# Kernel tuning notes

Measured on AMD Instinct MI355X. Metric: run time of the kernel, lower is better.

The kernel has to match this reference:

```python
import jax, jax.numpy as jnp
import numpy as np

B, T, C, H = 4, 2048, 512, 8
HS = C // H  # head_size = 64
EPS = 1e-5


def layernorm(x, g, b):
    mu = jnp.mean(x, axis=-1, keepdims=True)
    var = jnp.mean(jnp.square(x - mu), axis=-1, keepdims=True)
    return (x - mu) * jax.lax.rsqrt(var + EPS) * g + b


def setup_inputs() -> dict:
    key = jax.random.key(0)
    ks = jax.random.split(key, 12)
    s_attn = 1.0 / np.sqrt(C)
    s_ff1 = 1.0 / np.sqrt(C)
    s_ff2 = 1.0 / np.sqrt(4 * C)
    return {
        "x": jax.random.normal(ks[0], (B, T, C), jnp.float32),
        "wq": jax.random.normal(ks[1], (H, C, HS), jnp.float32) * s_attn,
        "wk": jax.random.normal(ks[2], (H, C, HS), jnp.float32) * s_attn,
        "wv": jax.random.normal(ks[3], (H, C, HS), jnp.float32) * s_attn,
        "w1": jax.random.normal(ks[4], (C, 4 * C), jnp.float32) * s_ff1,
        "b1": jnp.zeros((4 * C,), jnp.float32),
        "w2": jax.random.normal(ks[5], (4 * C, C), jnp.float32) * s_ff2,
        "b2": jnp.zeros((C,), jnp.float32),
        "ln1_g": jnp.ones((C,), jnp.float32),
        "ln1_b": jnp.zeros((C,), jnp.float32),
        "ln2_g": jnp.ones((C,), jnp.float32),
        "ln2_b": jnp.zeros((C,), jnp.float32),
    }


def reference(x, wq, wk, wv, w1, b1, w2, b2, ln1_g, ln1_b, ln2_g, ln2_b):
    # pre-LN multi-head causal self-attention
    h = layernorm(x, ln1_g, ln1_b)                       # [B,T,C]
    q = jnp.einsum("btc,hcd->bhtd", h, wq)
    k = jnp.einsum("btc,hcd->bhtd", h, wk)
    v = jnp.einsum("btc,hcd->bhtd", h, wv)
    # NOTE: source scales by full embed dim C, not head_size
    scores = jnp.einsum("bhtd,bhsd->bhts", q, k) * (C ** -0.5)  # [B,H,T,T]
    causal = jnp.tril(jnp.ones((T, T), bool))
    scores = jnp.where(causal, scores, -jnp.inf)
    att = jax.nn.softmax(scores, axis=-1)
    out = jnp.einsum("bhts,bhsd->bhtd", att, v)          # [B,H,T,HS]
    out = out.transpose(0, 2, 1, 3).reshape(B, T, C)     # concat heads
    x = x + out
    # FFN with residual
    h2 = layernorm(x, ln2_g, ln2_b)
    ff = jax.nn.relu(h2 @ w1 + b1) @ w2 + b2
    return x + ff
```

## Files before the change

kernel.cpp:

```cpp
#include <hip/hip_runtime.h>

typedef unsigned short ushort_t;
typedef __attribute__((ext_vector_type(8))) short short8;
typedef __attribute__((ext_vector_type(4))) float floatx4;

#define B_  4
#define T_  2048
#define C_  512
#define H_  8
#define HS_ 64
#define M_  (B_*T_)
#define SCALE2 0.06376140168547404f

__device__ __forceinline__ float b2f(ushort_t u) {
  union { unsigned int i; float f; } w; w.i = ((unsigned int)u) << 16; return w.f;
}
__device__ __forceinline__ ushort_t f2b(float f) {
  union { float f; unsigned int i; } w; w.f = f;
  unsigned int x = w.i;
  return (ushort_t)((x + 0x7fffu + ((x >> 16) & 1u)) >> 16);
}
__device__ __forceinline__ unsigned int cvtpk(float a, float b) {
  unsigned int r;
  asm("v_cvt_pk_bf16_f32 %0, %1, %2" : "=v"(r) : "v"(a), "v"(b));
  return r;
}
__device__ __forceinline__ void gl_lds16(const ushort_t* g, ushort_t* l) {
  __builtin_amdgcn_global_load_lds((const unsigned int*)g, (unsigned int*)l, 16, 0, 0);
}

__global__ __launch_bounds__(256) void transpose_all(const float* __restrict__ wq,
                                                     const float* __restrict__ wk,
                                                     const float* __restrict__ wv,
                                                     const float* __restrict__ w1,
                                                     const float* __restrict__ w2,
                                                     ushort_t* __restrict__ qkvt,
                                                     ushort_t* __restrict__ w1t,
                                                     ushort_t* __restrict__ w2t) {
  __shared__ ushort_t t[32][33];
  int idx = blockIdx.x;
  const float* in; ushort_t* out; int K, N, bx, by, z = 0;
  float scl = (idx < 256) ? SCALE2 : 1.0f;
  if (idx < 768) {
    int seg = idx >> 8, li = idx & 255;
    in = seg == 0 ? wq : (seg == 1 ? wk : wv);
    out = qkvt + (size_t)seg * 262144;
    K = 512; N = 64;
    z = li >> 5; li &= 31;
    bx = li & 1; by = li >> 1;
  } else if (idx < 1792) {
    int li = idx - 768;
    in = w1; out = w1t; K = 512; N = 2048;
    bx = li & 63; by = li >> 6;
  } else {
    int li = idx - 1792;
    in = w2; out = w2t; K = 2048; N = 512;
    bx = li & 15; by = li >> 4;
  }
  size_t zoff = (size_t)z * K * N;
  int n0 = bx * 32, k0 = by * 32;
  int tx = threadIdx.x & 31, ty = threadIdx.x >> 5;
#pragma unroll
  for (int i = 0; i < 4; i++)
    t[ty + 8 * i][tx] = f2b(in[zoff + (size_t)(k0 + ty + 8 * i) * N + n0 + tx] * scl);
  __syncthreads();
#pragma unroll
  for (int i = 0; i < 4; i++)
    out[zoff + (size_t)(n0 + ty + 8 * i) * K + k0 + tx] = t[tx][ty + 8 * i];
}

__global__ __launch_bounds__(256) void ln_k(const float* __restrict__ X,
                                            const float* __restrict__ g,
                                            const float* __restrict__ bb,
                                            ushort_t* __restrict__ Y) {
  int wave = threadIdx.x >> 6, lane = threadIdx.x & 63;
  size_t row = (size_t)blockIdx.x * 4 + wave;
  float v[8], s = 0.f, s2 = 0.f;
#pragma unroll
  for (int i = 0; i < 8; i++) {
    float x = X[row * C_ + lane + 64 * i];
    v[i] = x; s += x; s2 += x * x;
  }
#pragma unroll
  for (int off = 32; off >= 1; off >>= 1) {
    s += __shfl_xor(s, off); s2 += __shfl_xor(s2, off);
  }
  float mu = s * (1.0f / C_);
  float var = s2 * (1.0f / C_) - mu * mu;
  float rs = rsqrtf(var + 1e-5f);
  ushort_t* yr = Y + row * C_;
#pragma unroll
  for (int i = 0; i < 8; i++) {
    int c = lane + 64 * i;
    yr[c] = f2b((v[i] - mu) * rs * g[c] + bb[c]);
  }
}

__global__ __launch_bounds__(256) void gemm_bt128(const ushort_t* __restrict__ A,
                                                  const ushort_t* __restrict__ Bt,
                                                  ushort_t* __restrict__ Out,
                                                  int K, int ldOut,
                                                  const float* __restrict__ bias,
                                                  int relu) {
  __shared__ __align__(16) ushort_t As[128 * 64];
  __shared__ __align__(16) ushort_t Bs[128 * 64];
  const int tid = threadIdx.x;
  const int lane = tid & 63, wave = tid >> 6;
  const long row0 = (long)blockIdx.x * 128;
  const long col0 = (long)blockIdx.y * 128;
  const int srow = wave * 32 + (lane >> 3);
  const int scol = (((lane & 7) ^ ((lane >> 3) & 7))) * 8;
  const ushort_t* Ab = A + (size_t)(row0 + srow) * K + scol;
  const ushort_t* Bb = Bt + (size_t)(col0 + srow) * K + scol;
  const int wm = (wave >> 1) * 64, wn = (wave & 1) * 64;
  const int fq = lane >> 4, fl = lane & 15;
  floatx4 acc[4][4] = {};

  for (int k0 = 0; k0 < K; k0 += 64) {
    __syncthreads();
#pragma unroll
    for (int i = 0; i < 4; i++) {
      gl_lds16(Ab + (size_t)(i * 8) * K + k0, &As[(wave * 32 + i * 8) * 64]);
      gl_lds16(Bb + (size_t)(i * 8) * K + k0, &Bs[(wave * 32 + i * 8) * 64]);
    }
    __syncthreads();
#pragma unroll
    for (int ks = 0; ks < 2; ks++) {
      short8 af[4], bf[4];
      const int sl = ((ks * 4 + fq) ^ (fl & 7)) * 8;
#pragma unroll
      for (int i = 0; i < 4; i++) {
        af[i] = *(const short8*)&As[(wm + i * 16 + fl) * 64 + sl];
        bf[i] = *(const short8*)&Bs[(wn + i * 16 + fl) * 64 + sl];
      }
#pragma unroll
      for (int fi = 0; fi < 4; fi++)
#pragma unroll
        for (int fj = 0; fj < 4; fj++)
          acc[fi][fj] = __builtin_amdgcn_mfma_f32_16x16x32_bf16(af[fi], bf[fj], acc[fi][fj], 0, 0, 0);
    }
  }
#pragma unroll
  for (int fi = 0; fi < 4; fi++)
#pragma unroll
    for (int fj = 0; fj < 4; fj++) {
      long gcol = col0 + wn + fj * 16 + fl;
      float bv = bias ? bias[gcol] : 0.0f;
#pragma unroll
      for (int r = 0; r < 4; r++) {
        long grow = row0 + wm + fi * 16 + fq * 4 + r;
        float v = acc[fi][fj][r] + bv;
        if (relu) v = fmaxf(v, 0.0f);
        Out[(size_t)grow * ldOut + gcol] = f2b(v);
      }
    }
}

__global__ __launch_bounds__(256) void gemm_bt64(const ushort_t* __restrict__ A,
                                                 const ushort_t* __restrict__ Bt,
                                                 float* __restrict__ Out,
                                                 int K, int ldOut,
                                                 const float* __restrict__ bias,
                                                 const float* __restrict__ residual) {
  __shared__ __align__(16) ushort_t As[64 * 64];
  __shared__ __align__(16) ushort_t Bs[64 * 64];
  const int tid = threadIdx.x;
  const int lane = tid & 63, wave = tid >> 6;
  const long row0 = (long)blockIdx.x * 64;
  const long col0 = (long)blockIdx.y * 64;
  const int srow = wave * 16 + (lane >> 3);
  const int scol = (((lane & 7) ^ ((lane >> 3) & 7))) * 8;
  const ushort_t* Ab = A + (size_t)(row0 + srow) * K + scol;
  const ushort_t* Bb = Bt + (size_t)(col0 + srow) * K + scol;
  const int wm = (wave >> 1) * 32, wn = (wave & 1) * 32;
  const int fq = lane >> 4, fl = lane & 15;
  floatx4 acc[2][2] = {};

  for (int k0 = 0; k0 < K; k0 += 64) {
    __syncthreads();
#pragma unroll
    for (int i = 0; i < 2; i++) {
      gl_lds16(Ab + (size_t)(i * 8) * K + k0, &As[(wave * 16 + i * 8) * 64]);
      gl_lds16(Bb + (size_t)(i * 8) * K + k0, &Bs[(wave * 16 + i * 8) * 64]);
    }
    __syncthreads();
#pragma unroll
    for (int ks = 0; ks < 2; ks++) {
      short8 af[2], bf[2];
      const int sl = ((ks * 4 + fq) ^ (fl & 7)) * 8;
#pragma unroll
      for (int i = 0; i < 2; i++) {
        af[i] = *(const short8*)&As[(wm + i * 16 + fl) * 64 + sl];
        bf[i] = *(const short8*)&Bs[(wn + i * 16 + fl) * 64 + sl];
      }
#pragma unroll
      for (int fi = 0; fi < 2; fi++)
#pragma unroll
        for (int fj = 0; fj < 2; fj++)
          acc[fi][fj] = __builtin_amdgcn_mfma_f32_16x16x32_bf16(af[fi], bf[fj], acc[fi][fj], 0, 0, 0);
    }
  }
#pragma unroll
  for (int fi = 0; fi < 2; fi++)
#pragma unroll
    for (int fj = 0; fj < 2; fj++) {
      long gcol = col0 + wn + fj * 16 + fl;
      float bv = bias[gcol];
#pragma unroll
      for (int r = 0; r < 4; r++) {
        long grow = row0 + wm + fi * 16 + fq * 4 + r;
        size_t oi = (size_t)grow * ldOut + gcol;
        Out[oi] = acc[fi][fj][r] + bv + residual[oi];
      }
    }
}

__global__ __launch_bounds__(512) void flash_attn(const ushort_t* __restrict__ QKV,
                                                  const float* __restrict__ X,
                                                  float* __restrict__ X1) {
  __shared__ __align__(16) ushort_t kt[2][64 * 72];
  __shared__ __align__(16) ushort_t vt[2][64 * 72];
  const int tid = threadIdx.x;
  const int lane = tid & 63, wave = tid >> 6;
  const int fq = lane >> 4, fl = lane & 15;
  const int g = blockIdx.x >> 5;
  const int tile = g < 8 ? 15 - g : g - 8;
  const int bh = blockIdx.x & 31;
  const int h = bh & 7, b = bh >> 3;
  const int hoff = h * HS_;
  const int q0 = tile * 128;
  const int LD = 3 * C_;
  const int nst = 2 * tile + 2;
  const int whalf = wave >> 2;
  const int qg = q0 + wave * 16 + fl;

  short8 qf0, qf1;
  {
    const ushort_t* qp = QKV + (size_t)((size_t)b * T_ + q0 + wave * 16 + fl) * LD + hoff + fq * 8;
    qf0 = *(const short8*)(qp);
    qf1 = *(const short8*)(qp + 32);
  }
  short8 of;
  {
    short ob = (fl == 0) ? (short)0x3F80 : (short)0;
#pragma unroll
    for (int i = 0; i < 8; i++) of[i] = ob;
  }
  floatx4 oacc[4] = {};
  floatx4 lacc = {};

  const int role = tid >> 8;
  const int t2 = tid & 255;
  const int sr2 = (t2 >> 3) * 2;
  const int d0 = (t2 & 7) * 8;
  const ushort_t* sbase = QKV + (size_t)((size_t)b * T_ + sr2) * LD + hoff +
                          (role ? C_ : 2 * C_);

  const int addrA = ((2 * (fq & 1)) * 16 + fl) * 4;
  const int addrB = addrA + 64;
  const bool lowq = fq < 2;

  short8 r0 = *(const short8*)(sbase + d0);
  short8 r1 = *(const short8*)(sbase + LD + d0);
  if (role) {
    *(short8*)&kt[0][sr2 * 72 + d0] = r0;
    *(short8*)&kt[0][(sr2 + 1) * 72 + d0] = r1;
  } else {
#pragma unroll
    for (int i = 0; i < 8; i++) {
      int d = d0 + i;
      int scol = sr2 ^ (8 * (d >> 3));
      unsigned int pk = ((unsigned int)(ushort_t)r0[i]) |
                        (((unsigned int)(ushort_t)r1[i]) << 16);
      *(unsigned int*)&vt[0][d * 72 + scol] = pk;
    }
  }
  {
    const ushort_t* sp = sbase + (size_t)64 * LD;
    r0 = *(const short8*)(sp + d0);
    r1 = *(const short8*)(sp + LD + d0);
  }

  for (int st = 0; st < nst; st++) {
    __syncthreads();
    const int cur = st & 1;
    if (st + 1 < nst) {
      const int nb = cur ^ 1;
      if (role) {
        *(short8*)&kt[nb][sr2 * 72 + d0] = r0;
        *(short8*)&kt[nb][(sr2 + 1) * 72 + d0] = r1;
      } else {
#pragma unroll
        for (int i = 0; i < 8; i++) {
          int d = d0 + i;
          int scol = sr2 ^ (8 * (d >> 3));
          unsigned int pk = ((unsigned int)(ushort_t)r0[i]) |
                            (((unsigned int)(ushort_t)r1[i]) << 16);
          *(unsigned int*)&vt[nb][d * 72 + scol] = pk;
        }
      }
      if (st + 2 < nst) {
        const ushort_t* sp = sbase + (size_t)(st + 2) * 64 * LD;
        r0 = *(const short8*)(sp + d0);
        r1 = *(const short8*)(sp + LD + d0);
      }
    }

    if (!(whalf == 0 && st == nst - 1)) {
      const int s0 = st * 64;
      floatx4 sacc[4] = {};
#pragma unroll
      for (int fn = 0; fn < 4; fn++) {
        short8 kf0 = *(const short8*)&kt[cur][(fn * 16 + fl) * 72 + fq * 8];
        short8 kf1 = *(const short8*)&kt[cur][(fn * 16 + fl) * 72 + 32 + fq * 8];
        sacc[fn] = __builtin_amdgcn_mfma_f32_16x16x32_bf16(kf0, qf0, sacc[fn], 0, 0, 0);
        sacc[fn] = __builtin_amdgcn_mfma_f32_16x16x32_bf16(kf1, qf1, sacc[fn], 0, 0, 0);
      }
      const bool diag = (st == 2 * tile + whalf);
      unsigned int xc[4][2];
#pragma unroll
      for (int fn = 0; fn < 4; fn++) {
        float p[4];
#pragma unroll
        for (int r = 0; r < 4; r++) {
          float pv = exp2f(sacc[fn][r]);
          if (diag && (s0 + fn * 16 + fq * 4 + r) > qg) pv = 0.0f;
          p[r] = pv;
        }
        xc[fn][0] = cvtpk(p[0], p[1]);
        xc[fn][1] = cvtpk(p[2], p[3]);
      }
      union U8 { unsigned int u[4]; short8 s8; } pu[2];
#pragma unroll
      for (int o = 0; o < 2; o++)
#pragma unroll
        for (int t = 0; t < 4; t++) {
          int ad = (t >> 1) ? addrB : addrA;
          int lo = __builtin_amdgcn_ds_bpermute(ad, (int)xc[2 * o][t & 1]);
          int hi = __builtin_amdgcn_ds_bpermute(ad, (int)xc[2 * o + 1][t & 1]);
          pu[o].u[t] = lowq ? (unsigned int)lo : (unsigned int)hi;
        }
      short8 pf0 = pu[0].s8, pf1 = pu[1].s8;
#pragma unroll
      for (int fn = 0; fn < 4; fn++) {
        int drow = fn * 16 + fl;
        int sw = 8 * (drow >> 3);
        short8 vf0 = *(const short8*)&vt[cur][drow * 72 + ((fq * 8) ^ sw)];
        short8 vf1 = *(const short8*)&vt[cur][drow * 72 + ((32 + fq * 8) ^ sw)];
        oacc[fn] = __builtin_amdgcn_mfma_f32_16x16x32_bf16(pf0, vf0, oacc[fn], 0, 0, 0);
        oacc[fn] = __builtin_amdgcn_mfma_f32_16x16x32_bf16(pf1, vf1, oacc[fn], 0, 0, 0);
      }
      lacc = __builtin_amdgcn_mfma_f32_16x16x32_bf16(pf0, of, lacc, 0, 0, 0);
      lacc = __builtin_amdgcn_mfma_f32_16x16x32_bf16(pf1, of, lacc, 0, 0, 0);
    }
  }
#pragma unroll
  for (int r = 0; r < 4; r++) {
    float lr = __shfl(lacc[r], lane & 48);
    float inv = 1.0f / lr;
    int qgr = q0 + wave * 16 + fq * 4 + r;
#pragma unroll
    for (int fn = 0; fn < 4; fn++) {
      int d = fn * 16 + fl;
      size_t oi = ((size_t)b * T_ + qgr) * C_ + hoff + d;
      X1[oi] = oacc[fn][r] * inv + X[oi];
    }
  }
}

extern "C" void kernel_launch(void* const* d_in, const int* in_sizes, int n_in,
                              void* d_out, int out_size, void* d_ws, size_t ws_size,
                              hipStream_t stream) {
  const float* x  = (const float*)d_in[0];
  const float* wq = (const float*)d_in[1];
  const float* wk = (const float*)d_in[2];
  const float* wv = (const float*)d_in[3];
  const float* w1 = (const float*)d_in[4];
  const float* b1 = (const float*)d_in[5];
  const float* w2 = (const float*)d_in[6];
  const float* b2 = (const float*)d_in[7];
  const float* ln1g = (const float*)d_in[8];
  const float* ln1b = (const float*)d_in[9];
  const float* ln2g = (const float*)d_in[10];
  const float* ln2b = (const float*)d_in[11];
  ushort_t* ws = (ushort_t*)d_ws;

  const size_t SZ = (size_t)M_ * C_;
  ushort_t* qkvt = ws;
  ushort_t* w1t  = qkvt + 786432;
  ushort_t* w2t  = w1t + 1048576;
  ushort_t* qkv  = w2t + 1048576;
  ushort_t* h2   = qkv;
  ushort_t* ff1  = qkv + SZ;
  ushort_t* h    = (ushort_t*)d_out;
  float* x1      = (float*)d_out;
  float* outf    = (float*)d_out;

  transpose_all<<<2816, 256, 0, stream>>>(wq, wk, wv, w1, w2, qkvt, w1t, w2t);
  ln_k<<<M_ / 4, 256, 0, stream>>>(x, ln1g, ln1b, h);
  gemm_bt128<<<dim3(64, 12), 256, 0, stream>>>(h, qkvt, qkv, 512, 1536, nullptr, 0);
  flash_attn<<<B_ * H_ * (T_ / 128), 512, 0, stream>>>(qkv, x, x1);
  ln_k<<<M_ / 4, 256, 0, stream>>>(x1, ln2g, ln2b, h2);
  for (int p = 0; p < 2; p++) {
    const size_t roff = (size_t)p * 4096;
    gemm_bt128<<<dim3(32, 16), 256, 0, stream>>>(h2 + roff * C_, w1t, ff1,
                                                 512, 2048, b1, 1);
    gemm_bt64<<<dim3(64, 8), 256, 0, stream>>>(ff1, w2t, outf + roff * C_,
                                               2048, 512, b2, x1 + roff * C_);
  }
}
```

Before: 251.4 us.

## Split-K FFN down-projection with 128x128 tiles and atomic accumulation

Replaces the 64x64-tile second FFN GEMM with a 128x128-tile kernel that splits K=2048 into four 512-wide chunks along grid z. Each chunk adds its partial sums into the fp32 output with unsafeAtomicAdd. The residual-plus-bias initialisation of the output moves into the second layernorm kernel, which writes x1+b2 in place. The larger tile raises data reuse per block while keeping 512 blocks. The cost is extra atomic traffic to the output, and summation order becomes nondeterministic.

Result: slower. 275.7 us (+9.7%).

```diff
diff --git a/kernel.cpp b/kernel.cpp
--- a/kernel.cpp
+++ b/kernel.cpp
@@ -72,7 +72,9 @@
 __global__ __launch_bounds__(256) void ln_k(const float* __restrict__ X,
                                             const float* __restrict__ g,
                                             const float* __restrict__ bb,
-                                            ushort_t* __restrict__ Y) {
+                                            ushort_t* __restrict__ Y,
+                                            const float* __restrict__ badd,
+                                            float* __restrict__ Finit) {
   int wave = threadIdx.x >> 6, lane = threadIdx.x & 63;
   size_t row = (size_t)blockIdx.x * 4 + wave;
   float v[8], s = 0.f, s2 = 0.f;
@@ -93,6 +95,14 @@
   for (int i = 0; i < 8; i++) {
     int c = lane + 64 * i;
     yr[c] = f2b((v[i] - mu) * rs * g[c] + bb[c]);
+  }
+  if (Finit) {
+    float* fr = Finit + row * C_;
+#pragma unroll
+    for (int i = 0; i < 8; i++) {
+      int c = lane + 64 * i;
+      fr[c] = v[i] + badd[c];
+    }
   }
 }
 
@@ -156,61 +166,59 @@
     }
 }
 
-__global__ __launch_bounds__(256) void gemm_bt64(const ushort_t* __restrict__ A,
-                                                 const ushort_t* __restrict__ Bt,
-                                                 float* __restrict__ Out,
-                                                 int K, int ldOut,
-                                                 const float* __restrict__ bias,
-                                                 const float* __restrict__ residual) {
-  __shared__ __align__(16) ushort_t As[64 * 64];
-  __shared__ __align__(16) ushort_t Bs[64 * 64];
+__global__ __launch_bounds__(256) void gemm_bt128_atomic(const ushort_t* __restrict__ A,
+                                                         const ushort_t* __restrict__ Bt,
+                                                         float* __restrict__ Out,
+                                                         int Kc, int lda, int ldb,
+                                                         int ldOut) {
+  __shared__ __align__(16) ushort_t As[128 * 64];
+  __shared__ __align__(16) ushort_t Bs[128 * 64];
   const int tid = threadIdx.x;
   const int lane = tid & 63, wave = tid >> 6;
-  const long row0 = (long)blockIdx.x * 64;
-  const long col0 = (long)blockIdx.y * 64;
-  const int srow = wave * 16 + (lane >> 3);
+  const long row0 = (long)blockIdx.x * 128;
+  const long col0 = (long)blockIdx.y * 128;
+  const long koff = (long)blockIdx.z * Kc;
+  const int srow = wave * 32 + (lane >> 3);
   const int scol = (((lane & 7) ^ ((lane >> 3) & 7))) * 8;
-  const ushort_t* Ab = A + (size_t)(row0 + srow) * K + scol;
-  const ushort_t* Bb = Bt + (size_t)(col0 + srow) * K + scol;
-  const int wm = (wave >> 1) * 32, wn = (wave & 1) * 32;
+  const ushort_t* Ab = A + (size_t)(row0 + srow) * lda + koff + scol;
+  const ushort_t* Bb = Bt + (size_t)(col0 + srow) * ldb + koff + scol;
+  const int wm = (wave >> 1) * 64, wn = (wave & 1) * 64;
   const int fq = lane >> 4, fl = lane & 15;
-  floatx4 acc[2][2] = {};
-
-  for (int k0 = 0; k0 < K; k0 += 64) {
+  floatx4 acc[4][4] = {};
+
+  for (int k0 = 0; k0 < Kc; k0 += 64) {
     __syncthreads();
 #pragma unroll
-    for (int i = 0; i < 2; i++) {
-      gl_lds16(Ab + (size_t)(i * 8) * K + k0, &As[(wave * 16 + i * 8) * 64]);
-      gl_lds16(Bb + (size_t)(i * 8) * K + k0, &Bs[(wave * 16 + i * 8) * 64]);
+    for (int i = 0; i < 4; i++) {
+      gl_lds16(Ab + (size_t)(i * 8) * lda + k0, &As[(wave * 32 + i * 8) * 64]);
+      gl_lds16(Bb + (size_t)(i * 8) * ldb + k0, &Bs[(wave * 32 + i * 8) * 64]);
     }
     __syncthreads();
 #pragma unroll
     for (int ks = 0; ks < 2; ks++) {
-      short8 af[2], bf[2];
+      short8 af[4], bf[4];
       const int sl = ((ks * 4 + fq) ^ (fl & 7)) * 8;
 #pragma unroll
-      for (int i = 0; i < 2; i++) {
+      for (int i = 0; i < 4; i++) {
         af[i] = *(const short8*)&As[(wm + i * 16 + fl) * 64 + sl];
         bf[i] = *(const short8*)&Bs[(wn + i * 16 + fl) * 64 + sl];
       }
 #pragma unroll
-      for (int fi = 0; fi < 2; fi++)
-#pragma unroll
-        for (int fj = 0; fj < 2; fj++)
+      for (int fi = 0; fi < 4; fi++)
+#pragma unroll
+        for (int fj = 0; fj < 4; fj++)
           acc[fi][fj] = __builtin_amdgcn_mfma_f32_16x16x32_bf16(af[fi], bf[fj], acc[fi][fj], 0, 0, 0);
     }
   }
 #pragma unroll
-  for (int fi = 0; fi < 2; fi++)
-#pragma unroll
-    for (int fj = 0; fj < 2; fj++) {
+  for (int fi = 0; fi < 4; fi++)
+#pragma unroll
+    for (int fj = 0; fj < 4; fj++) {
       long gcol = col0 + wn + fj * 16 + fl;
-      float bv = bias[gcol];
 #pragma unroll
       for (int r = 0; r < 4; r++) {
         long grow = row0 + wm + fi * 16 + fq * 4 + r;
-        size_t oi = (size_t)grow * ldOut + gcol;
-        Out[oi] = acc[fi][fj][r] + bv + residual[oi];
+        unsafeAtomicAdd(&Out[(size_t)grow * ldOut + gcol], acc[fi][fj][r]);
       }
     }
 }
@@ -397,15 +405,15 @@
   float* outf    = (float*)d_out;
 
   transpose_all<<<2816, 256, 0, stream>>>(wq, wk, wv, w1, w2, qkvt, w1t, w2t);
-  ln_k<<<M_ / 4, 256, 0, stream>>>(x, ln1g, ln1b, h);
+  ln_k<<<M_ / 4, 256, 0, stream>>>(x, ln1g, ln1b, h, nullptr, nullptr);
   gemm_bt128<<<dim3(64, 12), 256, 0, stream>>>(h, qkvt, qkv, 512, 1536, nullptr, 0);
   flash_attn<<<B_ * H_ * (T_ / 128), 512, 0, stream>>>(qkv, x, x1);
-  ln_k<<<M_ / 4, 256, 0, stream>>>(x1, ln2g, ln2b, h2);
+  ln_k<<<M_ / 4, 256, 0, stream>>>(x1, ln2g, ln2b, h2, b2, outf);
   for (int p = 0; p < 2; p++) {
     const size_t roff = (size_t)p * 4096;
     gemm_bt128<<<dim3(32, 16), 256, 0, stream>>>(h2 + roff * C_, w1t, ff1,
                                                  512, 2048, b1, 1);
-    gemm_bt64<<<dim3(64, 8), 256, 0, stream>>>(ff1, w2t, outf + roff * C_,
-                                               2048, 512, b2, x1 + roff * C_);
-  }
-}
+    gemm_bt128_atomic<<<dim3(32, 4, 4), 256, 0, stream>>>(ff1, w2t, outf + roff * C_,
+                                                          512, 2048, 2048, 512);
+  }
+}
```

## Shrink flash attention query tile to 64 rows with 4-wave blocks

Applied to the files above, without the earlier changes.

Each flash-attention block now handles 64 query rows with 256 threads instead of 128 rows with 512 threads, so the grid doubles to 1024 blocks. Each loader thread now stages four K/V rows per step instead of two, and the special-case masking of the last step for the lower half of the waves goes away. The aim is finer-grained scheduling, better load balance across compute units on the causal triangle, and less wasted work on the diagonal. The cost is that each K/V tile is reused by fewer query rows, which raises shared-memory fill traffic and global loads per unit of compute.

After: 245.5 us. -2.3%, faster.

```diff
diff --git a/kernel.cpp b/kernel.cpp
--- a/kernel.cpp
+++ b/kernel.cpp
@@ -215,7 +215,7 @@
     }
 }
 
-__global__ __launch_bounds__(512) void flash_attn(const ushort_t* __restrict__ QKV,
+__global__ __launch_bounds__(256) void flash_attn(const ushort_t* __restrict__ QKV,
                                                   const float* __restrict__ X,
                                                   float* __restrict__ X1) {
   __shared__ __align__(16) ushort_t kt[2][64 * 72];
@@ -224,14 +224,13 @@
   const int lane = tid & 63, wave = tid >> 6;
   const int fq = lane >> 4, fl = lane & 15;
   const int g = blockIdx.x >> 5;
-  const int tile = g < 8 ? 15 - g : g - 8;
+  const int tile = g < 16 ? 31 - g : g - 16;
   const int bh = blockIdx.x & 31;
   const int h = bh & 7, b = bh >> 3;
   const int hoff = h * HS_;
-  const int q0 = tile * 128;
+  const int q0 = tile * 64;
   const int LD = 3 * C_;
-  const int nst = 2 * tile + 2;
-  const int whalf = wave >> 2;
+  const int nst = tile + 1;
   const int qg = q0 + wave * 16 + fl;
 
   short8 qf0, qf1;
@@ -249,11 +248,11 @@
   floatx4 oacc[4] = {};
   floatx4 lacc = {};
 
-  const int role = tid >> 8;
-  const int t2 = tid & 255;
-  const int sr2 = (t2 >> 3) * 2;
+  const int role = tid >> 7;
+  const int t2 = tid & 127;
+  const int sr4 = (t2 >> 3) * 4;
   const int d0 = (t2 & 7) * 8;
-  const ushort_t* sbase = QKV + (size_t)((size_t)b * T_ + sr2) * LD + hoff +
+  const ushort_t* sbase = QKV + (size_t)((size_t)b * T_ + sr4) * LD + hoff +
                           (role ? C_ : 2 * C_);
 
   const int addrA = ((2 * (fq & 1)) * 16 + fl) * 4;
@@ -262,23 +261,32 @@
 
   short8 r0 = *(const short8*)(sbase + d0);
   short8 r1 = *(const short8*)(sbase + LD + d0);
+  short8 r2 = *(const short8*)(sbase + 2 * LD + d0);
+  short8 r3 = *(const short8*)(sbase + 3 * LD + d0);
   if (role) {
-    *(short8*)&kt[0][sr2 * 72 + d0] = r0;
-    *(short8*)&kt[0][(sr2 + 1) * 72 + d0] = r1;
+    *(short8*)&kt[0][sr4 * 72 + d0] = r0;
+    *(short8*)&kt[0][(sr4 + 1) * 72 + d0] = r1;
+    *(short8*)&kt[0][(sr4 + 2) * 72 + d0] = r2;
+    *(short8*)&kt[0][(sr4 + 3) * 72 + d0] = r3;
   } else {
 #pragma unroll
     for (int i = 0; i < 8; i++) {
       int d = d0 + i;
-      int scol = sr2 ^ (8 * (d >> 3));
-      unsigned int pk = ((unsigned int)(ushort_t)r0[i]) |
-                        (((unsigned int)(ushort_t)r1[i]) << 16);
-      *(unsigned int*)&vt[0][d * 72 + scol] = pk;
+      int scol = sr4 ^ (8 * (d >> 3));
+      unsigned int pkA = ((unsigned int)(ushort_t)r0[i]) |
+                         (((unsigned int)(ushort_t)r1[i]) << 16);
+      unsigned int pkB = ((unsigned int)(ushort_t)r2[i]) |
+                         (((unsigned int)(ushort_t)r3[i]) << 16);
+      *(unsigned int*)&vt[0][d * 72 + scol] = pkA;
+      *(unsigned int*)&vt[0][d * 72 + scol + 2] = pkB;
     }
   }
   {
     const ushort_t* sp = sbase + (size_t)64 * LD;
     r0 = *(const short8*)(sp + d0);
     r1 = *(const short8*)(sp + LD + d0);
+    r2 = *(const short8*)(sp + 2 * LD + d0);
+    r3 = *(const short8*)(sp + 3 * LD + d0);
   }
 
   for (int st = 0; st < nst; st++) {
@@ -287,26 +295,33 @@
     if (st + 1 < nst) {
       const int nb = cur ^ 1;
       if (role) {
-        *(short8*)&kt[nb][sr2 * 72 + d0] = r0;
-        *(short8*)&kt[nb][(sr2 + 1) * 72 + d0] = r1;
+        *(short8*)&kt[nb][sr4 * 72 + d0] = r0;
+        *(short8*)&kt[nb][(sr4 + 1) * 72 + d0] = r1;
+        *(short8*)&kt[nb][(sr4 + 2) * 72 + d0] = r2;
+        *(short8*)&kt[nb][(sr4 + 3) * 72 + d0] = r3;
       } else {
 #pragma unroll
         for (int i = 0; i < 8; i++) {
           int d = d0 + i;
-          int scol = sr2 ^ (8 * (d >> 3));
-          unsigned int pk = ((unsigned int)(ushort_t)r0[i]) |
-                            (((unsigned int)(ushort_t)r1[i]) << 16);
-          *(unsigned int*)&vt[nb][d * 72 + scol] = pk;
+          int scol = sr4 ^ (8 * (d >> 3));
+          unsigned int pkA = ((unsigned int)(ushort_t)r0[i]) |
+                             (((unsigned int)(ushort_t)r1[i]) << 16);
+          unsigned int pkB = ((unsigned int)(ushort_t)r2[i]) |
+                             (((unsigned int)(ushort_t)r3[i]) << 16);
+          *(unsigned int*)&vt[nb][d * 72 + scol] = pkA;
+          *(unsigned int*)&vt[nb][d * 72 + scol + 2] = pkB;
         }
       }
       if (st + 2 < nst) {
         const ushort_t* sp = sbase + (size_t)(st + 2) * 64 * LD;
         r0 = *(const short8*)(sp + d0);
         r1 = *(const short8*)(sp + LD + d0);
-      }
-    }
-
-    if (!(whalf == 0 && st == nst - 1)) {
+        r2 = *(const short8*)(sp + 2 * LD + d0);
+        r3 = *(const short8*)(sp + 3 * LD + d0);
+      }
+    }
+
+    {
       const int s0 = st * 64;
       floatx4 sacc[4] = {};
 #pragma unroll
@@ -316,7 +331,7 @@
         sacc[fn] = __builtin_amdgcn_mfma_f32_16x16x32_bf16(kf0, qf0, sacc[fn], 0, 0, 0);
         sacc[fn] = __builtin_amdgcn_mfma_f32_16x16x32_bf16(kf1, qf1, sacc[fn], 0, 0, 0);
       }
-      const bool diag = (st == 2 * tile + whalf);
+      const bool diag = (st == tile);
       unsigned int xc[4][2];
 #pragma unroll
       for (int fn = 0; fn < 4; fn++) {
@@ -399,7 +414,7 @@
   transpose_all<<<2816, 256, 0, stream>>>(wq, wk, wv, w1, w2, qkvt, w1t, w2t);
   ln_k<<<M_ / 4, 256, 0, stream>>>(x, ln1g, ln1b, h);
   gemm_bt128<<<dim3(64, 12), 256, 0, stream>>>(h, qkvt, qkv, 512, 1536, nullptr, 0);
-  flash_attn<<<B_ * H_ * (T_ / 128), 512, 0, stream>>>(qkv, x, x1);
+  flash_attn<<<B_ * H_ * (T_ / 64), 256, 0, stream>>>(qkv, x, x1);
   ln_k<<<M_ / 4, 256, 0, stream>>>(x1, ln2g, ln2b, h2);
   for (int p = 0; p < 2; p++) {
     const size_t roff = (size_t)p * 4096;
```
